# Kernel tuning notes

Measured on AMD Instinct MI355X. Metric: run time of the kernel, lower is better.

## Reference

```python
import jax, jax.numpy as jnp
import numpy as np


def log_g(x):
    # log of g(x) = x + 0.5 if x >= 0 else sigmoid(x)  (minGRU paper Appendix B)
    return jnp.where(x >= 0, jnp.log(jax.nn.relu(x) + 0.5), -jax.nn.softplus(-x))


def parallel_scan_log(log_coeffs, log_values):
    # log_coeffs: [B, T, H]; log_values: [B, T+1, H]
    a_star = jnp.pad(jnp.cumsum(log_coeffs, axis=1), ((0, 0), (1, 0), (0, 0)))  # [B, T+1, H]
    log_h = a_star + jax.lax.cumlogsumexp(log_values - a_star, axis=1)
    return jnp.exp(log_h)  # [B, T+1, H]


def setup_inputs() -> dict:
    key = jax.random.key(0)
    ks = jax.random.split(key, 6)
    B, T, D, H = 4, 4096, 1024, 1024
    scale = 1.0 / np.sqrt(D)
    return {
        "x": jax.random.normal(ks[0], (B, T, D), dtype=jnp.float32),
        "h_0": jax.random.uniform(ks[1], (B, H), dtype=jnp.float32),
        "Wz": jax.random.normal(ks[2], (H, D), dtype=jnp.float32) * scale,
        "bz": jnp.zeros((H,), dtype=jnp.float32),
        "Wh": jax.random.normal(ks[3], (H, D), dtype=jnp.float32) * scale,
        "bh": jnp.zeros((H,), dtype=jnp.float32),
    }


def reference(x, h_0, Wz, bz, Wh, bh):
    T = x.shape[1]
    k = jnp.einsum("btd,hd->bth", x, Wz) + bz          # linear_z(x)
    log_z = -jax.nn.softplus(-k)                          # log sigmoid(k)
    log_coeffs = -jax.nn.softplus(k)                      # log (1 - sigmoid(k))
    log_h_0 = log_g(h_0)[:, None, :]                      # [B, 1, H]
    log_tilde_h = log_g(jnp.einsum("btd,hd->bth", x, Wh) + bh)
    log_values = jnp.concatenate([log_h_0, log_z + log_tilde_h], axis=1)  # [B, T+1, H]
    h = parallel_scan_log(log_coeffs, log_values)
    return h[:, -T:, :]
```

## Files before the change

### kernel.cpp

```cpp
#include <hip/hip_runtime.h>
#include <hip/hip_bf16.h>
#include <hip/hip_fp16.h>

#define B_ 4
#define T_ 4096
#define D_ 1024
#define H_ 1024
#define M_ (B_ * T_)

typedef __attribute__((ext_vector_type(8))) short short8;
typedef __attribute__((ext_vector_type(4))) float f32x4;

__device__ __forceinline__ unsigned short f2bf(float f) {
    unsigned int u = __float_as_uint(f);
    u += 0x7fffu + ((u >> 16) & 1u);
    return (unsigned short)(u >> 16);
}

__global__ __launch_bounds__(256) void convert_all(
    const float* __restrict__ x, const float* __restrict__ wz, const float* __restrict__ wh,
    unsigned short* __restrict__ xb, unsigned short* __restrict__ wzb, unsigned short* __restrict__ whb)
{
    int i = blockIdx.x * 256 + threadIdx.x;
    const float* s; unsigned short* d; int off;
    if (i < 4194304)      { s = x;  d = xb;  off = i; }
    else if (i < 4456448) { s = wz; d = wzb; off = i - 4194304; }
    else                  { s = wh; d = whb; off = i - 4456448; }
    float4 f = ((const float4*)s)[off];
    ushort4 u;
    u.x = f2bf(f.x); u.y = f2bf(f.y); u.z = f2bf(f.z); u.w = f2bf(f.w);
    ((ushort4*)d)[off] = u;
}

__device__ __forceinline__ void async16(const void* g, void* l) {
    __builtin_amdgcn_global_load_lds(
        (__attribute__((address_space(1))) void*)g,
        (__attribute__((address_space(3))) void*)l,
        16, 0, 0);
}

__global__ __launch_bounds__(256, 4) void dual_gemm_kernel(
    const unsigned short* __restrict__ xb,
    const unsigned short* __restrict__ wzb,
    const unsigned short* __restrict__ whb,
    const float* __restrict__ bz,
    const float* __restrict__ bh,
    __half2* __restrict__ av16,
    float2* __restrict__ chunkAV)
{
    __shared__ short8 ldsA[8 * 64];
    __shared__ short8 ldsBz[4 * 64];
    __shared__ short8 ldsBh[4 * 64];

    const int tid   = threadIdx.x;
    const int lane  = tid & 63;
    const int w     = __builtin_amdgcn_readfirstlane(tid >> 6);
    const int whalf = w >> 1;
    const int nhalf = w & 1;
    const int nb    = blockIdx.x >> 7;
    const int mb    = blockIdx.x & 127;
    const int r16   = lane & 15;
    const int q     = lane >> 4;

    const int laneoff = r16 * D_ + q * 8;

    const unsigned short* gA0 = xb  + (size_t)(mb * 128 + (2 * w) * 16) * D_ + laneoff;
    const unsigned short* gA1 = gA0 + 16 * D_;
    const unsigned short* gBz = wzb + (size_t)(nb * 64 + w * 16) * D_ + laneoff;
    const unsigned short* gBh = whb + (size_t)(nb * 64 + w * 16) * D_ + laneoff;
    short8* lA0 = &ldsA[(2 * w) * 64];
    short8* lA1 = &ldsA[(2 * w + 1) * 64];
    short8* lBz = &ldsBz[w * 64];
    short8* lBh = &ldsBh[w * 64];

    f32x4 accz[4][2] = {};
    f32x4 acch[4][2] = {};

    for (int kk = 0; kk < D_; kk += 32) {
        __syncthreads();
        async16(gA0 + kk, lA0);
        async16(gA1 + kk, lA1);
        async16(gBz + kk, lBz);
        async16(gBh + kk, lBh);
        __syncthreads();

        short8 fa[4], fz[2], fh[2];
#pragma unroll
        for (int gm = 0; gm < 4; ++gm) fa[gm] = ldsA[(whalf * 4 + gm) * 64 + lane];
#pragma unroll
        for (int gn = 0; gn < 2; ++gn) {
            fz[gn] = ldsBz[(nhalf * 2 + gn) * 64 + lane];
            fh[gn] = ldsBh[(nhalf * 2 + gn) * 64 + lane];
        }
#pragma unroll
        for (int gm = 0; gm < 4; ++gm)
#pragma unroll
            for (int gn = 0; gn < 2; ++gn) {
                accz[gm][gn] = __builtin_amdgcn_mfma_f32_16x16x32_bf16(fa[gm], fz[gn], accz[gm][gn], 0, 0, 0);
                acch[gm][gn] = __builtin_amdgcn_mfma_f32_16x16x32_bf16(fa[gm], fh[gn], acch[gm][gn], 0, 0, 0);
            }
    }

    const int cglob = mb * 2 + whalf;
    const int cc = cglob & 63;
    const int bb = cglob >> 6;
#pragma unroll
    for (int gn = 0; gn < 2; ++gn) {
        const int ncol = nb * 64 + nhalf * 32 + gn * 16 + r16;
        const float bzv = bz[ncol];
        const float bhv = bh[ncol];
        float CA = 1.0f, CV = 0.0f;
#pragma unroll
        for (int gm = 0; gm < 4; ++gm) {
            float LA = 1.0f, LV = 0.0f;
#pragma unroll
            for (int rr = 0; rr < 4; ++rr) {
                float kv = accz[gm][gn][rr] + bzv;
                float hv = acch[gm][gn][rr] + bhv;
                float tk = __expf(-fabsf(kv));
                float ik = 1.0f / (1.0f + tk);
                float sig = (kv >= 0.0f) ? ik : tk * ik;
                float ac  = (kv >= 0.0f) ? tk * ik : ik;
                float th = __expf(-fabsf(hv));
                float ih = 1.0f / (1.0f + th);
                float gh = (hv >= 0.0f) ? (hv + 0.5f) : th * ih;
                float vv = sig * gh;
                const size_t m = (size_t)mb * 128 + whalf * 64 + gm * 16 + q * 4 + rr;
                av16[(size_t)m * H_ + ncol] = __floats2half2_rn(ac, vv);
                LV = ac * LV + vv;
                LA = ac * LA;
            }
#pragma unroll
            for (int mask = 16; mask <= 32; mask <<= 1) {
                float PA = __shfl_xor(LA, mask);
                float PV = __shfl_xor(LV, mask);
                if (lane & mask) { LV = LA * PV + LV; LA = LA * PA; }
                else             { LV = PA * LV + PV; LA = PA * LA; }
            }
            CV = LA * CV + LV;
            CA = LA * CA;
        }
        if (q == 0)
            chunkAV[cc * 4096 + bb * 1024 + ncol] = make_float2(CA, CV);
    }
}

__global__ __launch_bounds__(256) void scan_pass2(const float2* __restrict__ chunkAV,
                                                  const float* __restrict__ h0,
                                                  float* __restrict__ hstart) {
    int chan = blockIdx.x * blockDim.x + threadIdx.x;
    int n = chan & (H_ - 1);
    int b = chan >> 10;
    float x = h0[b * H_ + n];
    float h;
    if (x >= 0.0f) { h = x + 0.5f; }
    else { float t = __expf(x); h = t / (1.0f + t); }
#pragma unroll 8
    for (int c = 0; c < 64; ++c) {
        hstart[c * 4096 + chan] = h;
        float2 s = chunkAV[c * 4096 + chan];
        h = s.x * h + s.y;
    }
}

__global__ __launch_bounds__(256) void scan_pass3(const __half2* __restrict__ av16,
                                                  const float* __restrict__ hstart,
                                                  float* __restrict__ out) {
    int g = blockIdx.x * blockDim.x + threadIdx.x;
    int n = g & (H_ - 1);
    int rest = g >> 10;
    int c = rest & 63;
    int b = rest >> 6;
    float h = hstart[c * 4096 + b * 1024 + n];
    const __half2* base = av16 + ((size_t)(b * T_ + c * 64)) * H_ + n;
    float* obase = out + ((size_t)(b * T_ + c * 64)) * H_ + n;
#pragma unroll 8
    for (int t = 0; t < 64; ++t) {
        float2 p = __half22float2(base[(size_t)t * H_]);
        h = p.x * h + p.y;
        obase[(size_t)t * H_] = h;
    }
}

extern "C" void kernel_launch(void* const* d_in, const int* in_sizes, int n_in,
                              void* d_out, int out_size, void* d_ws, size_t ws_size,
                              hipStream_t stream) {
    const float* x  = (const float*)d_in[0];
    const float* h0 = (const float*)d_in[1];
    const float* Wz = (const float*)d_in[2];
    const float* bz = (const float*)d_in[3];
    const float* Wh = (const float*)d_in[4];
    const float* bh = (const float*)d_in[5];
    float* out = (float*)d_out;

    char* ws = (char*)d_ws;
    unsigned short* xb  = (unsigned short*)(ws);
    unsigned short* wzb = (unsigned short*)(ws + 33554432);
    unsigned short* whb = (unsigned short*)(ws + 35651584);
    __half2* av16       = (__half2*)(ws + 37748736);
    float2* chunkAV     = (float2*)(ws + 104857600);
    float*  hstart      = (float*)(ws + 106954752);

    convert_all<<<18432, 256, 0, stream>>>(x, Wz, Wh, xb, wzb, whb);

    dual_gemm_kernel<<<2048, 256, 0, stream>>>(xb, wzb, whb, bz, bh, av16, chunkAV);

    scan_pass2<<<16,   256, 0, stream>>>(chunkAV, h0, hstart);
    scan_pass3<<<1024, 256, 0, stream>>>(av16, hstart, out);
}
```

Baseline: 288.3 us.

## Enlarge dual GEMM tile with interleaved weights and double-buffered async pipeline

```diff
diff --git a/kernel.cpp b/kernel.cpp
--- a/kernel.cpp
+++ b/kernel.cpp
@@ -19,17 +19,27 @@
 
 __global__ __launch_bounds__(256) void convert_all(
     const float* __restrict__ x, const float* __restrict__ wz, const float* __restrict__ wh,
-    unsigned short* __restrict__ xb, unsigned short* __restrict__ wzb, unsigned short* __restrict__ whb)
+    unsigned short* __restrict__ xb, unsigned short* __restrict__ wcb)
 {
     int i = blockIdx.x * 256 + threadIdx.x;
-    const float* s; unsigned short* d; int off;
-    if (i < 4194304)      { s = x;  d = xb;  off = i; }
-    else if (i < 4456448) { s = wz; d = wzb; off = i - 4194304; }
-    else                  { s = wh; d = whb; off = i - 4456448; }
-    float4 f = ((const float4*)s)[off];
+    const float* s; unsigned short* d; int soff; int doff;
+    if (i < 4194304) {
+        s = x; d = xb; soff = i; doff = i;
+    } else if (i < 4456448) {
+        int off = i - 4194304;
+        int j = off >> 8; int k4 = off & 255;
+        int ic = ((j >> 4) << 5) + (j & 15);
+        s = wz; d = wcb; soff = off; doff = ic * 256 + k4;
+    } else {
+        int off = i - 4456448;
+        int j = off >> 8; int k4 = off & 255;
+        int ic = ((j >> 4) << 5) + 16 + (j & 15);
+        s = wh; d = wcb; soff = off; doff = ic * 256 + k4;
+    }
+    float4 f = ((const float4*)s)[soff];
     ushort4 u;
     u.x = f2bf(f.x); u.y = f2bf(f.y); u.z = f2bf(f.z); u.w = f2bf(f.w);
-    ((ushort4*)d)[off] = u;
+    ((ushort4*)d)[doff] = u;
 }
 
 __device__ __forceinline__ void async16(const void* g, void* l) {
@@ -39,110 +49,165 @@
         16, 0, 0);
 }
 
-__global__ __launch_bounds__(256, 4) void dual_gemm_kernel(
+#define BARRIER() do { asm volatile("" ::: "memory"); __builtin_amdgcn_s_barrier(); asm volatile("" ::: "memory"); } while (0)
+#define VMW(n)    asm volatile("s_waitcnt vmcnt(" #n ")" ::: "memory")
+
+__global__ __launch_bounds__(512, 2) void dual_gemm_kernel(
     const unsigned short* __restrict__ xb,
-    const unsigned short* __restrict__ wzb,
-    const unsigned short* __restrict__ whb,
+    const unsigned short* __restrict__ wcb,
     const float* __restrict__ bz,
     const float* __restrict__ bh,
     __half2* __restrict__ av16,
     float2* __restrict__ chunkAV)
 {
-    __shared__ short8 ldsA[8 * 64];
-    __shared__ short8 ldsBz[4 * 64];
-    __shared__ short8 ldsBh[4 * 64];
-
-    const int tid   = threadIdx.x;
-    const int lane  = tid & 63;
-    const int w     = __builtin_amdgcn_readfirstlane(tid >> 6);
-    const int whalf = w >> 1;
-    const int nhalf = w & 1;
-    const int nb    = blockIdx.x >> 7;
-    const int mb    = blockIdx.x & 127;
-    const int r16   = lane & 15;
-    const int q     = lane >> 4;
+    __shared__ short8 ldsA[2 * 2 * 16 * 64];
+    __shared__ short8 ldsB[2 * 2 * 16 * 64];
+
+    const int tid  = threadIdx.x;
+    const int lane = tid & 63;
+    const int w    = __builtin_amdgcn_readfirstlane(tid >> 6);
+    const int wr   = w >> 2;
+    const int wc   = w & 3;
+    const int r16  = lane & 15;
+    const int q    = lane >> 4;
+
+    const int bid = blockIdx.x;
+    const int swz = (bid & 7) * 64 + (bid >> 3);
+    const int nb  = swz & 7;
+    const int mb  = swz >> 3;
 
     const int laneoff = r16 * D_ + q * 8;
-
-    const unsigned short* gA0 = xb  + (size_t)(mb * 128 + (2 * w) * 16) * D_ + laneoff;
-    const unsigned short* gA1 = gA0 + 16 * D_;
-    const unsigned short* gBz = wzb + (size_t)(nb * 64 + w * 16) * D_ + laneoff;
-    const unsigned short* gBh = whb + (size_t)(nb * 64 + w * 16) * D_ + laneoff;
-    short8* lA0 = &ldsA[(2 * w) * 64];
-    short8* lA1 = &ldsA[(2 * w + 1) * 64];
-    short8* lBz = &ldsBz[w * 64];
-    short8* lBh = &ldsBh[w * 64];
-
-    f32x4 accz[4][2] = {};
-    f32x4 acch[4][2] = {};
-
-    for (int kk = 0; kk < D_; kk += 32) {
-        __syncthreads();
-        async16(gA0 + kk, lA0);
-        async16(gA1 + kk, lA1);
-        async16(gBz + kk, lBz);
-        async16(gBh + kk, lBh);
-        __syncthreads();
-
-        short8 fa[4], fz[2], fh[2];
-#pragma unroll
-        for (int gm = 0; gm < 4; ++gm) fa[gm] = ldsA[(whalf * 4 + gm) * 64 + lane];
-#pragma unroll
-        for (int gn = 0; gn < 2; ++gn) {
-            fz[gn] = ldsBz[(nhalf * 2 + gn) * 64 + lane];
-            fh[gn] = ldsBh[(nhalf * 2 + gn) * 64 + lane];
-        }
-#pragma unroll
-        for (int gm = 0; gm < 4; ++gm)
-#pragma unroll
-            for (int gn = 0; gn < 2; ++gn) {
-                accz[gm][gn] = __builtin_amdgcn_mfma_f32_16x16x32_bf16(fa[gm], fz[gn], accz[gm][gn], 0, 0, 0);
-                acch[gm][gn] = __builtin_amdgcn_mfma_f32_16x16x32_bf16(fa[gm], fh[gn], acch[gm][gn], 0, 0, 0);
-            }
-    }
-
-    const int cglob = mb * 2 + whalf;
-    const int cc = cglob & 63;
-    const int bb = cglob >> 6;
-#pragma unroll
-    for (int gn = 0; gn < 2; ++gn) {
-        const int ncol = nb * 64 + nhalf * 32 + gn * 16 + r16;
+    const unsigned short* gA = xb  + (size_t)(mb * 256 + 2 * w * 16) * D_ + laneoff;
+    const unsigned short* gB = wcb + (size_t)(nb * 256 + 2 * w * 16) * D_ + laneoff;
+
+#define STAGE_A(tt, kh, pp) do { \
+    const unsigned short* _s = gA + (tt) * 64 + (kh) * 32; \
+    short8* _d = &ldsA[(pp) * 2048 + (kh) * 1024 + 2 * w * 64]; \
+    async16(_s, _d); \
+    async16(_s + 16 * D_, _d + 64); } while (0)
+#define STAGE_B(tt, kh, pp) do { \
+    const unsigned short* _s = gB + (tt) * 64 + (kh) * 32; \
+    short8* _d = &ldsB[(pp) * 2048 + (kh) * 1024 + 2 * w * 64]; \
+    async16(_s, _d); \
+    async16(_s + 16 * D_, _d + 64); } while (0)
+
+    f32x4 acc[8][4] = {};
+
+    STAGE_A(0, 0, 0); STAGE_B(0, 0, 0);
+    STAGE_A(0, 1, 0); STAGE_B(0, 1, 0);
+    STAGE_A(1, 0, 1); STAGE_B(1, 0, 1);
+    VMW(8);
+    BARRIER();
+
+    short8 fa[4], fb[4];
+
+#define MFMA16(MH) do { \
+    _Pragma("unroll") \
+    for (int m = 0; m < 4; ++m) { \
+        _Pragma("unroll") \
+        for (int n = 0; n < 4; ++n) \
+            acc[(MH) * 4 + m][n] = __builtin_amdgcn_mfma_f32_16x16x32_bf16( \
+                fa[m], fb[n], acc[(MH) * 4 + m][n], 0, 0, 0); \
+    } } while (0)
+
+    for (int g = 0; g < 16; ++g) {
+        const int p  = g & 1;
+        const int bA = p * 2048;
+        const int oA = bA + wr * 512;
+        const int oB = bA + wc * 256;
+
+#pragma unroll
+        for (int m = 0; m < 4; ++m) fa[m] = ldsA[oA + m * 64 + lane];
+#pragma unroll
+        for (int n = 0; n < 4; ++n) fb[n] = ldsB[oB + n * 64 + lane];
+        if (g < 15) STAGE_A(g + 1, 1, p ^ 1);
+        BARRIER();
+        __builtin_amdgcn_s_setprio(1);
+        MFMA16(0);
+        __builtin_amdgcn_s_setprio(0);
+        BARRIER();
+
+#pragma unroll
+        for (int m = 0; m < 4; ++m) fa[m] = ldsA[oA + (4 + m) * 64 + lane];
+        if (g < 15) STAGE_B(g + 1, 1, p ^ 1);
+        BARRIER();
+        __builtin_amdgcn_s_setprio(1);
+        MFMA16(1);
+        __builtin_amdgcn_s_setprio(0);
+        if (g < 15) { VMW(8); } else { VMW(0); }
+        BARRIER();
+
+#pragma unroll
+        for (int m = 0; m < 4; ++m) fa[m] = ldsA[oA + 1024 + m * 64 + lane];
+#pragma unroll
+        for (int n = 0; n < 4; ++n) fb[n] = ldsB[oB + 1024 + n * 64 + lane];
+        if (g < 14) STAGE_A(g + 2, 0, p);
+        BARRIER();
+        __builtin_amdgcn_s_setprio(1);
+        MFMA16(0);
+        __builtin_amdgcn_s_setprio(0);
+        BARRIER();
+
+#pragma unroll
+        for (int m = 0; m < 4; ++m) fa[m] = ldsA[oA + 1024 + (4 + m) * 64 + lane];
+        if (g < 14) STAGE_B(g + 2, 0, p);
+        BARRIER();
+        __builtin_amdgcn_s_setprio(1);
+        MFMA16(1);
+        __builtin_amdgcn_s_setprio(0);
+        if (g < 14) { VMW(8); } else if (g == 14) { VMW(4); }
+        BARRIER();
+    }
+
+    const int mrow0 = mb * 256 + wr * 128;
+#pragma unroll
+    for (int gg = 0; gg < 2; ++gg) {
+        const int ncol = nb * 128 + wc * 32 + gg * 16 + r16;
         const float bzv = bz[ncol];
         const float bhv = bh[ncol];
-        float CA = 1.0f, CV = 0.0f;
-#pragma unroll
-        for (int gm = 0; gm < 4; ++gm) {
-            float LA = 1.0f, LV = 0.0f;
-#pragma unroll
-            for (int rr = 0; rr < 4; ++rr) {
-                float kv = accz[gm][gn][rr] + bzv;
-                float hv = acch[gm][gn][rr] + bhv;
-                float tk = __expf(-fabsf(kv));
-                float ik = 1.0f / (1.0f + tk);
-                float sig = (kv >= 0.0f) ? ik : tk * ik;
-                float ac  = (kv >= 0.0f) ? tk * ik : ik;
-                float th = __expf(-fabsf(hv));
-                float ih = 1.0f / (1.0f + th);
-                float gh = (hv >= 0.0f) ? (hv + 0.5f) : th * ih;
-                float vv = sig * gh;
-                const size_t m = (size_t)mb * 128 + whalf * 64 + gm * 16 + q * 4 + rr;
-                av16[(size_t)m * H_ + ncol] = __floats2half2_rn(ac, vv);
-                LV = ac * LV + vv;
-                LA = ac * LA;
+#pragma unroll
+        for (int hh = 0; hh < 2; ++hh) {
+            float CA = 1.0f, CV = 0.0f;
+#pragma unroll
+            for (int mm = 0; mm < 4; ++mm) {
+                const int mf = hh * 4 + mm;
+                float LA = 1.0f, LV = 0.0f;
+#pragma unroll
+                for (int rr = 0; rr < 4; ++rr) {
+                    float kv = acc[mf][2 * gg + 0][rr] + bzv;
+                    float hv = acc[mf][2 * gg + 1][rr] + bhv;
+                    float tk = __expf(-fabsf(kv));
+                    float ik = 1.0f / (1.0f + tk);
+                    float sig = (kv >= 0.0f) ? ik : tk * ik;
+                    float ac  = (kv >= 0.0f) ? tk * ik : ik;
+                    float th = __expf(-fabsf(hv));
+                    float ih = 1.0f / (1.0f + th);
+                    float gh = (hv >= 0.0f) ? (hv + 0.5f) : th * ih;
+                    float vv = sig * gh;
+                    const size_t m = (size_t)(mrow0 + mf * 16 + q * 4 + rr);
+                    av16[m * H_ + ncol] = __floats2half2_rn(ac, vv);
+                    LV = ac * LV + vv;
+                    LA = ac * LA;
+                }
+#pragma unroll
+                for (int mask = 16; mask <= 32; mask <<= 1) {
+                    float PA = __shfl_xor(LA, mask);
+                    float PV = __shfl_xor(LV, mask);
+                    if (lane & mask) { LV = LA * PV + LV; LA = LA * PA; }
+                    else             { LV = PA * LV + PV; LA = PA * LA; }
+                }
+                CV = LA * CV + LV;
+                CA = LA * CA;
             }
-#pragma unroll
-            for (int mask = 16; mask <= 32; mask <<= 1) {
-                float PA = __shfl_xor(LA, mask);
-                float PV = __shfl_xor(LV, mask);
-                if (lane & mask) { LV = LA * PV + LV; LA = LA * PA; }
-                else             { LV = PA * LV + PV; LA = PA * LA; }
+            if (q == 0) {
+                const int cglob = mb * 4 + wr * 2 + hh;
+                chunkAV[(cglob & 63) * 4096 + (cglob >> 6) * 1024 + ncol] = make_float2(CA, CV);
             }
-            CV = LA * CV + LV;
-            CA = LA * CA;
         }
-        if (q == 0)
-            chunkAV[cc * 4096 + bb * 1024 + ncol] = make_float2(CA, CV);
-    }
+    }
+#undef STAGE_A
+#undef STAGE_B
+#undef MFMA16
 }
 
 __global__ __launch_bounds__(256) void scan_pass2(const float2* __restrict__ chunkAV,
@@ -195,15 +260,14 @@
 
     char* ws = (char*)d_ws;
     unsigned short* xb  = (unsigned short*)(ws);
-    unsigned short* wzb = (unsigned short*)(ws + 33554432);
-    unsigned short* whb = (unsigned short*)(ws + 35651584);
+    unsigned short* wcb = (unsigned short*)(ws + 33554432);
     __half2* av16       = (__half2*)(ws + 37748736);
     float2* chunkAV     = (float2*)(ws + 104857600);
     float*  hstart      = (float*)(ws + 106954752);
 
-    convert_all<<<18432, 256, 0, stream>>>(x, Wz, Wh, xb, wzb, whb);
-
-    dual_gemm_kernel<<<2048, 256, 0, stream>>>(xb, wzb, whb, bz, bh, av16, chunkAV);
+    convert_all<<<18432, 256, 0, stream>>>(x, Wz, Wh, xb, wcb);
+
+    dual_gemm_kernel<<<512, 512, 0, stream>>>(xb, wcb, bz, bh, av16, chunkAV);
 
     scan_pass2<<<16,   256, 0, stream>>>(chunkAV, h0, hstart);
     scan_pass3<<<1024, 256, 0, stream>>>(av16, hstart, out);
```

Measured after the change: 273.3 us. 1.05x faster.
